# Kernel tuning notes

Hardware: AMD Instinct MI355X
Metric: run time of the kernel (lower is better)

The kernel has to match this reference:

```python
import jax, jax.numpy as jnp
import numpy as np

DIM = 1024
NUM_HEADS = 16
HEAD_DIM = 64
SCALE = 1.0 / np.sqrt(float(HEAD_DIM))


def setup_inputs() -> dict:
    key = jax.random.key(0)
    ks = jax.random.split(key, 11)
    B, S, D = 2, 4096, DIM
    glorot = lambda k, shape: jax.random.uniform(
        k, shape, jnp.float32,
        -jnp.sqrt(6.0 / (shape[0] + shape[1])), jnp.sqrt(6.0 / (shape[0] + shape[1])))
    return {
        "x": jax.random.normal(ks[0], (B, S, D), jnp.float32),
        "Wq": glorot(ks[1], (D, NUM_HEADS * HEAD_DIM)),
        "bq": jnp.zeros((NUM_HEADS * HEAD_DIM,), jnp.float32),
        "Wk": glorot(ks[2], (D, NUM_HEADS * HEAD_DIM)),
        "bk": jnp.zeros((NUM_HEADS * HEAD_DIM,), jnp.float32),
        "Wv": glorot(ks[3], (D, NUM_HEADS * HEAD_DIM)),
        "bv": jnp.zeros((NUM_HEADS * HEAD_DIM,), jnp.float32),
        "Wqt": glorot(ks[4], (D, D)),
        "bqt": jnp.zeros((D,), jnp.float32),
        "Wo": glorot(ks[5], (D, D)),
        "bo": jnp.zeros((D,), jnp.float32),
        "num_anchor_tokens": 512,
    }


def _split_heads(t):
    # [B, T, H*Dh] -> [B, H, T, Dh]
    B, T, _ = t.shape
    return t.reshape(B, T, NUM_HEADS, HEAD_DIM).transpose(0, 2, 1, 3)


def reference(x, Wq, bq, Wk, bk, Wv, bv, Wqt, bqt, Wo, bo, num_anchor_tokens):
    B, S, D = x.shape
    A = num_anchor_tokens  # static Python int
    anchors = x[:, :A, :]            # [B, A, D]
    queries = x[:, A:, :]            # [B, S-A, D]

    anchor_q = _split_heads(anchors @ Wq + bq)   # [B, H, A, Dh]
    anchor_k = _split_heads(anchors @ Wk + bk)   # [B, H, A, Dh]
    anchor_v = _split_heads(anchors @ Wv + bv)   # [B, H, A, Dh]
    query_q = _split_heads(queries @ Wqt + bqt)  # [B, H, S-A, Dh]

    combined_q = jnp.concatenate([anchor_q, query_q], axis=2)  # [B, H, S, Dh]
    scores = jnp.einsum("bhsd,bhad->bhsa", combined_q, anchor_k) * SCALE
    attn = jax.nn.softmax(scores, axis=-1)        # [B, H, S, A]
    out = jnp.einsum("bhsa,bhad->bhsd", attn, anchor_v)  # [B, H, S, Dh]
    out = out.transpose(0, 2, 1, 3).reshape(B, S, D)
    return out @ Wo + bo
```

## Files before the change

### kernel.cpp

```cpp
#include <hip/hip_runtime.h>
#include <hip/hip_bf16.h>
#include <math.h>
#include <stdint.h>

typedef _Float16 f16;
typedef _Float16 f16x8 __attribute__((ext_vector_type(8)));
typedef _Float16 f16x4 __attribute__((ext_vector_type(4)));
typedef float f32x4 __attribute__((ext_vector_type(4)));

#define DIM   1024
#define NH    16
#define HD    64
#define BB    2
#define SS    4096
#define AA    512
#define SCALE 0.125f
#define EXP_C1 0.18033688011112043f
#define EXP_C2 (-2.8853900817779268f)

#define GLOAD_LDS16(g, l)                                                                   \
  __builtin_amdgcn_global_load_lds((const __attribute__((address_space(1))) uint32_t*)(g),  \
                                   (__attribute__((address_space(3))) uint32_t*)(l), 16, 0, 0)

static const size_t OFF_XH  = 0;
static const size_t OFF_WT  = 8388608;
static const size_t OFF_QC  = OFF_WT + 5u*1048576u;
static const size_t OFF_KB  = OFF_QC + 8388608u;
static const size_t OFF_VT  = OFF_KB + 1048576u;
static const size_t OFF_AO  = OFF_VT + 1048576u;

__global__ __launch_bounds__(256) void prep_kernel(const float* __restrict__ x,
                                                   f16* __restrict__ xh,
                                                   const float* W0, const float* W1,
                                                   const float* W2, const float* W3,
                                                   const float* W4,
                                                   f16* T0, f16* T1, f16* T2, f16* T3, f16* T4) {
    __shared__ float tile[32][33];
    const int bid = blockIdx.x;
    const int t   = threadIdx.x;
    if (bid < 8192) {
        size_t i = ((size_t)bid * 256 + t) * 4;
        float4 v = *reinterpret_cast<const float4*>(x + i);
        f16x4 o;
        o[0] = (f16)v.x; o[1] = (f16)v.y; o[2] = (f16)v.z; o[3] = (f16)v.w;
        *reinterpret_cast<f16x4*>(xh + i) = o;
        return;
    }
    const int bid2 = bid - 8192;
    const float* W; f16* T;
    switch (bid2 >> 10) {
        case 0: W = W0; T = T0; break;
        case 1: W = W1; T = T1; break;
        case 2: W = W2; T = T2; break;
        case 3: W = W3; T = T3; break;
        default: W = W4; T = T4; break;
    }
    const int rem = bid2 & 1023;
    const int gx = (rem & 31) << 5, gy = (rem >> 5) << 5;
    const int tx = t & 31, ty = t >> 5;
#pragma unroll
    for (int i = 0; i < 32; i += 8)
        tile[ty + i][tx] = W[(size_t)(gy + ty + i) * DIM + gx + tx];
    __syncthreads();
#pragma unroll
    for (int i = 0; i < 32; i += 8)
        T[(size_t)(gx + ty + i) * DIM + gy + tx] = (f16)tile[tx][ty + i];
}

#define P_STAGE(buf, k0)                                               \
    {                                                                  \
        GLOAD_LDS16(Ap + (k0), &As[buf][wid << 9]);                    \
        GLOAD_LDS16(Bp + (k0), &Bs[buf][wid << 9]);                    \
        GLOAD_LDS16(Bp + (k0) + (size_t)64 * DIM,                      \
                    &Bs[buf][(wid << 9) + 2048]);                      \
    }

__global__ __launch_bounds__(256) void proj_kernel(const f16* __restrict__ xh,
                                                   const f16* __restrict__ wtq,
                                                   const f16* __restrict__ wtqt,
                                                   const f16* __restrict__ wtk,
                                                   const f16* __restrict__ wtv,
                                                   const float* __restrict__ bq,
                                                   const float* __restrict__ bqt,
                                                   const float* __restrict__ bk,
                                                   const float* __restrict__ bv,
                                                   f16* __restrict__ qc,
                                                   f16* __restrict__ kbuf,
                                                   f16* __restrict__ vtb) {
    __shared__ __align__(16) f16 As[2][2048];
    __shared__ __align__(16) f16 Bs[2][4096];

    const int t    = threadIdx.x;
    const int wid  = t >> 6;
    const int lane = t & 63;
    const int lr   = lane & 15;
    const int lg   = lane >> 4;
    const int x    = blockIdx.x, bc = blockIdx.y;

    int b, srow0, mode, sdim;
    const f16* Bt; const float* bias; f16* outp;
    if (x < 128) {
        b = x >> 6; srow0 = (x & 63) * 64;
        if (srow0 < 512) { Bt = wtq; bias = bq; } else { Bt = wtqt; bias = bqt; }
        mode = 0; sdim = SS; outp = qc;
    } else if (x < 144) {
        int y = x - 128; b = y >> 3; srow0 = (y & 7) * 64;
        Bt = wtk; bias = bk; mode = 0; sdim = AA; outp = kbuf;
    } else {
        int y = x - 144; b = y >> 3; srow0 = (y & 7) * 64;
        Bt = wtv; bias = bv; mode = 1; sdim = AA; outp = vtb;
    }

    const int srow = (wid << 4) + (lane >> 2);
    const int sch  = ((lane & 3) ^ ((lane >> 3) & 3)) << 3;
    const f16* Ap = xh + ((size_t)b * SS + srow0 + srow) * DIM + sch;
    const f16* Bp = Bt + ((size_t)(bc * 128 + srow)) * DIM + sch;

    const int wr = (wid >> 1) * 32;
    const int wc = (wid & 1) * 64;

    f32x4 acc[2][4] = {};

    P_STAGE(0, 0);
    __syncthreads();
    int cur = 0;
    for (int k0 = 0; k0 < DIM; k0 += 32) {
        if (k0 + 32 < DIM) P_STAGE(cur ^ 1, k0 + 32);
        f16x8 af[2], bf[4];
#pragma unroll
        for (int m = 0; m < 2; m++) {
            const int r = wr + m * 16 + lr;
            af[m] = *reinterpret_cast<const f16x8*>(&As[cur][r * 32 + ((lg ^ ((r >> 1) & 3)) << 3)]);
        }
#pragma unroll
        for (int n = 0; n < 4; n++) {
            const int r = wc + n * 16 + lr;
            bf[n] = *reinterpret_cast<const f16x8*>(&Bs[cur][r * 32 + ((lg ^ ((r >> 1) & 3)) << 3)]);
        }
#pragma unroll
        for (int m = 0; m < 2; m++)
#pragma unroll
            for (int n = 0; n < 4; n++)
                acc[m][n] = __builtin_amdgcn_mfma_f32_16x16x32_f16(af[m], bf[n], acc[m][n], 0, 0, 0);
        __syncthreads();
        cur ^= 1;
    }

#pragma unroll
    for (int m = 0; m < 2; m++) {
        const int row_local = wr + m * 16 + lg * 4;
#pragma unroll
        for (int n = 0; n < 4; n++) {
            const int c  = bc * 128 + wc + n * 16 + lr;
            const float bvv = bias[c];
            const int h = c >> 6, d = c & 63;
#pragma unroll
            for (int q = 0; q < 4; q++) {
                const int s_g = srow0 + row_local + q;
                const float val = acc[m][n][q] + bvv;
                if (mode == 0)
                    outp[(((size_t)(b * NH + h)) * sdim + s_g) * HD + d] = (f16)val;
                else
                    outp[(((size_t)(b * NH + h)) * HD + d) * AA + s_g] = (f16)val;
            }
        }
    }
}

#define G_STAGE64(buf, k0)                                                     \
    {                                                                          \
        _Pragma("unroll")                                                      \
        for (int i = 0; i < 4; i++) {                                          \
            GLOAD_LDS16(Ap + (k0) + (size_t)(i * 32) * DIM,                    \
                        &As[buf][i * 2048 + (wid << 9)]);                      \
            GLOAD_LDS16(Bp + (k0) + (size_t)(i * 32) * DIM,                    \
                        &Bs[buf][i * 2048 + (wid << 9)]);                      \
        }                                                                      \
    }

__global__ __launch_bounds__(256) void final_gemm(const f16* __restrict__ ao,
                                                  const f16* __restrict__ wto,
                                                  const float* __restrict__ bo,
                                                  float* __restrict__ out) {
    __shared__ __align__(16) f16 As[2][8192];
    __shared__ __align__(16) f16 Bs[2][8192];

    const int t    = threadIdx.x;
    const int wid  = t >> 6;
    const int lane = t & 63;
    const int lr   = lane & 15;
    const int lg   = lane >> 4;
    const int br   = blockIdx.x, bc = blockIdx.y;

    const int b     = br >> 5;
    const int srow0 = (br & 31) * 128;

    const int srow = (wid << 3) + (lane >> 3);
    const int sch  = ((lane & 7) ^ (lane >> 3)) << 3;
    const f16* Ap = ao + ((size_t)b * SS + srow0 + srow) * DIM + sch;
    const f16* Bp = wto + ((size_t)(bc * 128 + srow)) * DIM + sch;

    const int wr = (wid >> 1) * 64;
    const int wc = (wid & 1) * 64;

    f32x4 acc[4][4] = {};

    G_STAGE64(0, 0);
    __syncthreads();
    int cur = 0;
    for (int k0 = 0; k0 < DIM; k0 += 64) {
        if (k0 + 64 < DIM) G_STAGE64(cur ^ 1, k0 + 64);
#pragma unroll
        for (int ks = 0; ks < 2; ks++) {
            f16x8 af[4], bf[4];
#pragma unroll
            for (int m = 0; m < 4; m++) {
                const int r = wr + m * 16 + lr;
                af[m] = *reinterpret_cast<const f16x8*>(
                    &As[cur][r * 64 + ((((ks << 2) + lg) ^ (lr & 7)) << 3)]);
            }
#pragma unroll
            for (int n = 0; n < 4; n++) {
                const int r = wc + n * 16 + lr;
                bf[n] = *reinterpret_cast<const f16x8*>(
                    &Bs[cur][r * 64 + ((((ks << 2) + lg) ^ (lr & 7)) << 3)]);
            }
#pragma unroll
            for (int m = 0; m < 4; m++)
#pragma unroll
                for (int n = 0; n < 4; n++)
                    acc[m][n] = __builtin_amdgcn_mfma_f32_16x16x32_f16(af[m], bf[n], acc[m][n], 0, 0, 0);
        }
        __syncthreads();
        cur ^= 1;
    }

#pragma unroll
    for (int m = 0; m < 4; m++) {
        const int row_local = wr + m * 16 + lg * 4;
#pragma unroll
        for (int n = 0; n < 4; n++) {
            const int c  = bc * 128 + wc + n * 16 + lr;
            const float bvv = bo[c];
#pragma unroll
            for (int q = 0; q < 4; q++)
                out[((size_t)b * SS + srow0 + row_local + q) * DIM + c] = acc[m][n][q] + bvv;
        }
    }
}

__global__ __launch_bounds__(512) void attn_kernel(const f16* __restrict__ qc,
                                                   const f16* __restrict__ kb,
                                                   const f16* __restrict__ vt,
                                                   f16* __restrict__ ao) {
    __shared__ __align__(16) f16 Ks[2][64 * 64];
    __shared__ __align__(16) f16 Vs[2][64 * 64];
    __shared__ __align__(16) f16 Ps[8][16][64];

    const int t    = threadIdx.x;
    const int wid  = t >> 6;
    const int lane = t & 63;
    const int lr   = lane & 15;
    const int lg   = lane >> 4;
    const int qt   = blockIdx.x;
    const int h    = blockIdx.y;
    const int b    = blockIdx.z;
    const size_t bh = (size_t)b * NH + h;

    const int qrow = qt * 128 + wid * 16 + lr;
    const f16* qp = qc + (bh * SS + qrow) * HD + lg * 8;
    const f16x8 qa0 = *reinterpret_cast<const f16x8*>(qp);
    const f16x8 qa1 = *reinterpret_cast<const f16x8*>(qp + 32);

    const int sr = (wid << 3) + (lane >> 3);
    const f16* kg = kb + bh * (size_t)AA * HD;
    const f16* vg = vt + bh * (size_t)HD * AA;

    f32x4 acc[4] = {};
    float rsum[4] = {0.f, 0.f, 0.f, 0.f};

#define ATTN_STAGE(buf, a0)                                                          \
    {                                                                                \
        const int ck = (((lane & 7) ^ (sr & 7)) << 3);                               \
        GLOAD_LDS16(kg + (size_t)((a0) + sr) * HD + ck, &Ks[buf][(wid << 3) * 64]);  \
        GLOAD_LDS16(vg + (size_t)sr * AA + (a0) + ck,   &Vs[buf][(wid << 3) * 64]);  \
    }

    ATTN_STAGE(0, 0);
    asm volatile("s_waitcnt vmcnt(0)");
    __syncthreads();

    int cur = 0;
    for (int at = 0; at < AA / 64; ++at) {
        if (at < AA / 64 - 1) ATTN_STAGE(cur ^ 1, (at + 1) * 64);

        f32x4 s[4];
#pragma unroll
        for (int n = 0; n < 4; n++) {
            const int r = n * 16 + lr;
            const int x = r & 7;
            f16x8 kf0 = *reinterpret_cast<const f16x8*>(&Ks[cur][r * 64 + ((lg ^ x) << 3)]);
            f16x8 kf1 = *reinterpret_cast<const f16x8*>(&Ks[cur][r * 64 + (((lg + 4) ^ x) << 3)]);
            f32x4 z = {};
            z = __builtin_amdgcn_mfma_f32_16x16x32_f16(qa0, kf0, z, 0, 0, 0);
            z = __builtin_amdgcn_mfma_f32_16x16x32_f16(qa1, kf1, z, 0, 0, 0);
            s[n] = z;
        }

#pragma unroll
        for (int n = 0; n < 4; n++) {
#pragma unroll
            for (int q = 0; q < 4; q++) {
                const float p = exp2f(fmaf(s[n][q], EXP_C1, EXP_C2));
                rsum[q] += p;
                const int row = lg * 4 + q;
                Ps[wid][row][(((2 * n + (lr >> 3)) ^ (row & 7)) << 3) + (lr & 7)] = (f16)p;
            }
        }
        const f16x8 pa0 = *reinterpret_cast<const f16x8*>(&Ps[wid][lr][(lg ^ (lr & 7)) << 3]);
        const f16x8 pa1 = *reinterpret_cast<const f16x8*>(&Ps[wid][lr][((lg + 4) ^ (lr & 7)) << 3]);

#pragma unroll
        for (int n = 0; n < 4; n++) {
            const int d = n * 16 + lr;
            const int x = d & 7;
            f16x8 vf0 = *reinterpret_cast<const f16x8*>(&Vs[cur][d * 64 + ((lg ^ x) << 3)]);
            f16x8 vf1 = *reinterpret_cast<const f16x8*>(&Vs[cur][d * 64 + (((lg + 4) ^ x) << 3)]);
            acc[n] = __builtin_amdgcn_mfma_f32_16x16x32_f16(pa0, vf0, acc[n], 0, 0, 0);
            acc[n] = __builtin_amdgcn_mfma_f32_16x16x32_f16(pa1, vf1, acc[n], 0, 0, 0);
        }

        if (at < AA / 64 - 1) {
            asm volatile("s_waitcnt vmcnt(0)");
            __syncthreads();
        }
        cur ^= 1;
    }

#pragma unroll
    for (int off = 1; off < 16; off <<= 1) {
#pragma unroll
        for (int q = 0; q < 4; q++) rsum[q] += __shfl_xor(rsum[q], off);
    }
#pragma unroll
    for (int q = 0; q < 4; q++) {
        const float inv = 1.0f / rsum[q];
        const int row = qt * 128 + wid * 16 + lg * 4 + q;
#pragma unroll
        for (int n = 0; n < 4; n++) {
            ao[((size_t)b * SS + row) * DIM + h * HD + n * 16 + lr] = (f16)(acc[n][q] * inv);
        }
    }
}

extern "C" void kernel_launch(void* const* d_in, const int* in_sizes, int n_in,
                              void* d_out, int out_size, void* d_ws, size_t ws_size,
                              hipStream_t stream) {
    const float* x   = (const float*)d_in[0];
    const float* Wq  = (const float*)d_in[1];
    const float* bq  = (const float*)d_in[2];
    const float* Wk  = (const float*)d_in[3];
    const float* bk  = (const float*)d_in[4];
    const float* Wv  = (const float*)d_in[5];
    const float* bv  = (const float*)d_in[6];
    const float* Wqt = (const float*)d_in[7];
    const float* bqt = (const float*)d_in[8];
    const float* Wo  = (const float*)d_in[9];
    const float* bo  = (const float*)d_in[10];

    f16* ws   = (f16*)d_ws;
    f16* xh   = ws + OFF_XH;
    f16* wtq  = ws + OFF_WT;
    f16* wtk  = wtq + 1048576u;
    f16* wtv  = wtk + 1048576u;
    f16* wtqt = wtv + 1048576u;
    f16* wto  = wtqt + 1048576u;
    f16* qc   = ws + OFF_QC;
    f16* kbuf = ws + OFF_KB;
    f16* vtb  = ws + OFF_VT;
    f16* ao   = ws + OFF_AO;

    prep_kernel<<<8192 + 5120, 256, 0, stream>>>(x, xh, Wq, Wk, Wv, Wqt, Wo,
                                                 wtq, wtk, wtv, wtqt, wto);

    proj_kernel<<<dim3(160, 8), 256, 0, stream>>>(xh, wtq, wtqt, wtk, wtv,
                                                  bq, bqt, bk, bv, qc, kbuf, vtb);

    attn_kernel<<<dim3(32, NH, BB), 512, 0, stream>>>(qc, kbuf, vtb, ao);

    final_gemm<<<dim3(64, 8), 256, 0, stream>>>(ao, wto, bo, (float*)d_out);
}
```

Baseline: 116.6 us.

## Use triple-buffered LDS pipeline with partial vmcnt waits in GEMM kernels

The projection GEMM moves from double to triple LDS buffering, prefetching two K-tiles ahead. Both GEMMs replace __syncthreads with explicit s_waitcnt vmcnt(N) plus raw s_barrier, so each iteration waits only for the oldest tile's global-to-LDS loads rather than draining all outstanding loads. This keeps more memory traffic in flight behind the MFMA work. It costs more LDS in the projection kernel, and correctness depends on the hand-counted vmcnt values matching the number of loads each stage issues.

```diff
diff --git a/kernel.cpp b/kernel.cpp
--- a/kernel.cpp
+++ b/kernel.cpp
@@ -87,8 +87,8 @@
                                                    f16* __restrict__ qc,
                                                    f16* __restrict__ kbuf,
                                                    f16* __restrict__ vtb) {
-    __shared__ __align__(16) f16 As[2][2048];
-    __shared__ __align__(16) f16 Bs[2][4096];
+    __shared__ __align__(16) f16 As[3][2048];
+    __shared__ __align__(16) f16 Bs[3][4096];
 
     const int t    = threadIdx.x;
     const int wid  = t >> 6;
@@ -122,28 +122,42 @@
     f32x4 acc[2][4] = {};
 
     P_STAGE(0, 0);
-    __syncthreads();
-    int cur = 0;
-    for (int k0 = 0; k0 < DIM; k0 += 32) {
-        if (k0 + 32 < DIM) P_STAGE(cur ^ 1, k0 + 32);
+    P_STAGE(1, 32);
+
+    int cb = 0;
+    for (int kt = 0; kt < 32; ++kt) {
+        const int sb = (cb >= 1) ? cb - 1 : cb + 2;
+        if (kt + 2 < 32) {
+            P_STAGE(sb, (kt + 2) * 32);
+            asm volatile("s_waitcnt vmcnt(6)" ::: "memory");
+        } else if (kt + 1 < 32) {
+            asm volatile("s_waitcnt vmcnt(3)" ::: "memory");
+        } else {
+            asm volatile("s_waitcnt vmcnt(0)" ::: "memory");
+        }
+        __builtin_amdgcn_s_barrier();
+        __builtin_amdgcn_sched_barrier(0);
+
         f16x8 af[2], bf[4];
 #pragma unroll
         for (int m = 0; m < 2; m++) {
             const int r = wr + m * 16 + lr;
-            af[m] = *reinterpret_cast<const f16x8*>(&As[cur][r * 32 + ((lg ^ ((r >> 1) & 3)) << 3)]);
+            af[m] = *reinterpret_cast<const f16x8*>(&As[cb][r * 32 + ((lg ^ ((r >> 1) & 3)) << 3)]);
         }
 #pragma unroll
         for (int n = 0; n < 4; n++) {
             const int r = wc + n * 16 + lr;
-            bf[n] = *reinterpret_cast<const f16x8*>(&Bs[cur][r * 32 + ((lg ^ ((r >> 1) & 3)) << 3)]);
+            bf[n] = *reinterpret_cast<const f16x8*>(&Bs[cb][r * 32 + ((lg ^ ((r >> 1) & 3)) << 3)]);
         }
 #pragma unroll
         for (int m = 0; m < 2; m++)
 #pragma unroll
             for (int n = 0; n < 4; n++)
                 acc[m][n] = __builtin_amdgcn_mfma_f32_16x16x32_f16(af[m], bf[n], acc[m][n], 0, 0, 0);
-        __syncthreads();
-        cur ^= 1;
+
+        __builtin_amdgcn_sched_barrier(0);
+        __builtin_amdgcn_s_barrier();
+        cb = (cb >= 2) ? 0 : cb + 1;
     }
 
 #pragma unroll
@@ -206,10 +220,17 @@
     f32x4 acc[4][4] = {};
 
     G_STAGE64(0, 0);
-    __syncthreads();
     int cur = 0;
-    for (int k0 = 0; k0 < DIM; k0 += 64) {
-        if (k0 + 64 < DIM) G_STAGE64(cur ^ 1, k0 + 64);
+    for (int kt = 0; kt < 16; ++kt) {
+        if (kt + 1 < 16) {
+            G_STAGE64(cur ^ 1, (kt + 1) * 64);
+            asm volatile("s_waitcnt vmcnt(8)" ::: "memory");
+        } else {
+            asm volatile("s_waitcnt vmcnt(0)" ::: "memory");
+        }
+        __builtin_amdgcn_s_barrier();
+        __builtin_amdgcn_sched_barrier(0);
+
 #pragma unroll
         for (int ks = 0; ks < 2; ks++) {
             f16x8 af[4], bf[4];
@@ -231,7 +252,9 @@
                 for (int n = 0; n < 4; n++)
                     acc[m][n] = __builtin_amdgcn_mfma_f32_16x16x32_f16(af[m], bf[n], acc[m][n], 0, 0, 0);
         }
-        __syncthreads();
+
+        __builtin_amdgcn_sched_barrier(0);
+        __builtin_amdgcn_s_barrier();
         cur ^= 1;
     }
 
```

Result: slower. 130.2 us (+11.7%).
